# Kernel optimization log

Measured on AMD Instinct MI355X. Metric: run time of the kernel, lower is better.

The kernel has to match this reference:

```python
import jax, jax.numpy as jnp
import numpy as np

B, S, P = 2, 1024, 1024          # batch, new tokens, start_pos (cached prefix)
E, H, KV, HD = 2048, 32, 8, 64    # embed, heads, kv groups, head_dim
G = H // KV                       # group size = 4
THETA = 500000.0
CTX = P + S                       # cache/context length = 2048


def _rope_tables(start, seqlen):
    inv_freq = 1.0 / (THETA ** (jnp.arange(0, HD, 2, dtype=jnp.float32) / HD))
    pos = jnp.arange(start, start + seqlen, dtype=jnp.float32)
    freqs = jnp.outer(pos, inv_freq)              # [S, HD/2]
    emb = jnp.concatenate([freqs, freqs], axis=-1)  # [S, HD]
    return jnp.cos(emb), jnp.sin(emb)


def setup_inputs() -> dict:
    key = jax.random.key(0)
    ks = jax.random.split(key, 8)
    x = jax.random.normal(ks[0], (B, S, E), dtype=jnp.float32)
    cos1, sin1 = _rope_tables(P, S)
    cos = jnp.broadcast_to(cos1[None], (B, S, HD))
    sin = jnp.broadcast_to(sin1[None], (B, S, HD))
    # causal-with-offset additive mask: query i (global pos P+i) sees key j <= P+i
    qpos = P + jnp.arange(S)[:, None]
    kpos = jnp.arange(CTX)[None, :]
    mask = jnp.where(kpos <= qpos, 0.0, -1e9).astype(jnp.float32)[None, None]  # [1,1,S,CTX]
    cache_k = jax.random.normal(ks[1], (B, KV, CTX, HD), dtype=jnp.float32)
    cache_v = jax.random.normal(ks[2], (B, KV, CTX, HD), dtype=jnp.float32)
    sc = 0.02
    Wq = jax.random.normal(ks[3], (E, E), dtype=jnp.float32) * sc
    Wk = jax.random.normal(ks[4], (KV * HD, E), dtype=jnp.float32) * sc
    Wv = jax.random.normal(ks[5], (KV * HD, E), dtype=jnp.float32) * sc
    Wo = jax.random.normal(ks[6], (E, E), dtype=jnp.float32) * sc
    return {"x": x, "cos": cos, "sin": sin, "mask": mask,
            "cache_k": cache_k, "cache_v": cache_v,
            "Wq": Wq, "Wk": Wk, "Wv": Wv, "Wo": Wo, "start_pos": P}


def _rotate_half(t):
    t1, t2 = t[..., : HD // 2], t[..., HD // 2:]
    return jnp.concatenate([-t2, t1], axis=-1)


def _apply_rope(t, cos, sin):
    # t: [B, nh, S, HD]; cos/sin: [B, S, HD] -> unsqueeze head dim
    c = cos[:, None]
    s = sin[:, None]
    return t * c + _rotate_half(t) * s


def reference(x, cos, sin, mask, cache_k, cache_v, Wq, Wk, Wv, Wo, start_pos):
    b, s, e = x.shape
    q = (x @ Wq.T).reshape(b, s, H, HD).transpose(0, 2, 1, 3)    # [B,H,S,HD]
    k = (x @ Wk.T).reshape(b, s, KV, HD).transpose(0, 2, 1, 3)   # [B,KV,S,HD]
    v = (x @ Wv.T).reshape(b, s, KV, HD).transpose(0, 2, 1, 3)
    q = _apply_rope(q, cos, sin)
    k = _apply_rope(k, cos, sin)
    ck = cache_k.at[:, :, start_pos:start_pos + s].set(k)
    cv = cache_v.at[:, :, start_pos:start_pos + s].set(v)
    keys = ck[:, :, : start_pos + s]      # [B,KV,T,HD]
    vals = cv[:, :, : start_pos + s]
    # GQA without materializing repeated KV: view q as [B,KV,G,S,HD]
    qg = q.reshape(b, KV, G, s, HD)
    scores = jnp.einsum("bkgsh,bkth->bkgst", qg, keys) / jnp.sqrt(jnp.float32(HD))
    scores = scores + mask[:, :, None]    # broadcast mask over group dim
    probs = jax.nn.softmax(scores.astype(jnp.float32), axis=-1).astype(x.dtype)
    out = jnp.einsum("bkgst,bkth->bkgsh", probs, vals)            # [B,KV,G,S,HD]
    out = out.reshape(b, H, s, HD).transpose(0, 2, 1, 3).reshape(b, s, e)
    return out @ Wo.T
```

## Files before the change

kernel.cpp:

```cpp
#include <hip/hip_runtime.h>
#include <cstddef>

#define B   2
#define S   1024
#define PP  1024
#define CTX 2048
#define E   2048
#define H   32
#define KVH 8
#define HD  64
#define GQ  4
#define NQKV 3072

typedef short s4v  __attribute__((ext_vector_type(4)));
typedef short s8v  __attribute__((ext_vector_type(8)));
typedef float f4v  __attribute__((ext_vector_type(4)));

__device__ __forceinline__ short f2bf(float f) {
  union { float f; unsigned u; } v; v.f = f;
  unsigned r = v.u + 0x7fffu + ((v.u >> 16) & 1u);
  return (short)(r >> 16);
}
__device__ __forceinline__ float bf2f(short h) {
  union { unsigned u; float f; } v; v.u = ((unsigned)(unsigned short)h) << 16;
  return v.f;
}

__device__ __forceinline__ void gl_lds16(const void* g, void* l) {
  __builtin_amdgcn_global_load_lds((const __attribute__((address_space(1))) unsigned*)g,
                                   (__attribute__((address_space(3))) unsigned*)l, 16, 0, 0);
}

__global__ __launch_bounds__(256) void prep(const float* __restrict__ x,
                                            const float* __restrict__ Wq,
                                            const float* __restrict__ Wk,
                                            const float* __restrict__ Wv,
                                            const float* __restrict__ Wo,
                                            const float* __restrict__ ck,
                                            const float* __restrict__ cv,
                                            short* __restrict__ xb,
                                            short* __restrict__ wqkv,
                                            short* __restrict__ wob,
                                            short* __restrict__ keys,
                                            short* __restrict__ vt,
                                            float4* __restrict__ outz) {
  __shared__ short Ts[64][72];
  const int blk = blockIdx.x, tid = threadIdx.x;
  if (blk < 7168) {
    const float* s; short* d; int base;
    if (blk < 2048)      { s = x;  d = xb;             base = blk; }
    else if (blk < 4096) { s = Wq; d = wqkv;           base = blk - 2048; }
    else if (blk < 4608) { s = Wk; d = wqkv + 4194304; base = blk - 4096; }
    else if (blk < 5120) { s = Wv; d = wqkv + 5242880; base = blk - 4608; }
    else                 { s = Wo; d = wob;            base = blk - 5120; }
    int i = (base * 256 + tid) * 8;
    float4 a = *(const float4*)&s[i];
    float4 b = *(const float4*)&s[i + 4];
    s8v o;
    o[0]=f2bf(a.x); o[1]=f2bf(a.y); o[2]=f2bf(a.z); o[3]=f2bf(a.w);
    o[4]=f2bf(b.x); o[5]=f2bf(b.y); o[6]=f2bf(b.z); o[7]=f2bf(b.w);
    *(s8v*)&d[i] = o;
  } else if (blk < 7680) {
    int idx = (blk - 7168) * 256 + tid;
    int bkv = idx >> 13;
    int rem = idx & 8191;
    size_t off = (size_t)bkv * (CTX * HD) + (size_t)rem * 8;
    float4 a = *(const float4*)&ck[off];
    float4 b = *(const float4*)&ck[off + 4];
    s8v o;
    o[0]=f2bf(a.x); o[1]=f2bf(a.y); o[2]=f2bf(a.z); o[3]=f2bf(a.w);
    o[4]=f2bf(b.x); o[5]=f2bf(b.y); o[6]=f2bf(b.z); o[7]=f2bf(b.w);
    *(s8v*)&keys[off] = o;
  } else if (blk < 7936) {
    const int blk2 = blk - 7680;
    const int bkv = blk2 >> 4;
    const int p0  = (blk2 & 15) * 64;
    const float* src = cv + (size_t)bkv * CTX * HD + (size_t)p0 * HD;
    {
      int dq = tid & 15, kb = tid >> 4;
      float4 vv[4];
#pragma unroll
      for (int i = 0; i < 4; i++)
        vv[i] = *(const float4*)&src[(size_t)(kb * 4 + i) * HD + dq * 4];
#pragma unroll
      for (int j = 0; j < 4; j++) {
        s4v p;
        p[0]=f2bf(((const float*)&vv[0])[j]); p[1]=f2bf(((const float*)&vv[1])[j]);
        p[2]=f2bf(((const float*)&vv[2])[j]); p[3]=f2bf(((const float*)&vv[3])[j]);
        *(s4v*)&Ts[dq * 4 + j][kb * 4] = p;
      }
    }
    __syncthreads();
    {
      int d = tid >> 2, c = tid & 3;
      short* dst = vt + ((size_t)bkv * HD + d) * CTX + p0 + (c >> 1) * 32 + (c & 1) * 4;
#pragma unroll
      for (int j = 0; j < 4; j++) {
        s4v q4 = *(const s4v*)&Ts[d][c * 16 + j * 4];
        *(s4v*)&dst[j * 8] = q4;
      }
    }
  } else {
    int i0 = (blk - 7936) * 1024 + tid * 4;
#pragma unroll
    for (int j = 0; j < 4; j++) outz[i0 + j] = make_float4(0.f, 0.f, 0.f, 0.f);
  }
}

__global__ __launch_bounds__(256) void qkv_gemm(const short* __restrict__ A,
                                                const short* __restrict__ Bw,
                                                short* __restrict__ qb,
                                                short* __restrict__ ktmp,
                                                short* __restrict__ vt) {
  __shared__ short As[8192];
  __shared__ short Bs[8192];
  const int tid  = threadIdx.x;
  const int wv   = tid >> 6, lane = tid & 63;
  const int wm   = wv & 1, wn = wv >> 1;
  const int n16  = lane & 15, g = lane >> 4;
  const int m0   = blockIdx.y * 128, n0 = blockIdx.x * 128;
  const int K = 2048;

  const int rr = tid >> 3;
  const int cc = ((tid & 7) ^ (rr & 7)) * 8;
  const short* pA = A  + (size_t)(m0 + rr) * K + cc;
  const short* pB = Bw + (size_t)(n0 + rr) * K + cc;

  f4v acc[4][4] = {};
  for (int k0 = 0; k0 < K; k0 += 64) {
    __syncthreads();
#pragma unroll
    for (int st = 0; st < 4; st++) {
      gl_lds16(pA + (size_t)st * 32 * K, As + (st * 256 + wv * 64) * 8);
      gl_lds16(pB + (size_t)st * 32 * K, Bs + (st * 256 + wv * 64) * 8);
    }
    pA += 64; pB += 64;
    __syncthreads();

#pragma unroll
    for (int kk = 0; kk < 2; kk++) {
      s8v af[4], bf[4];
#pragma unroll
      for (int mt = 0; mt < 4; mt++)
        af[mt] = *(const s8v*)&As[(wm * 64 + mt * 16 + n16) * 64 + (((kk << 2) | g) ^ (n16 & 7)) * 8];
#pragma unroll
      for (int nt = 0; nt < 4; nt++)
        bf[nt] = *(const s8v*)&Bs[(wn * 64 + nt * 16 + n16) * 64 + (((kk << 2) | g) ^ (n16 & 7)) * 8];
#pragma unroll
      for (int mt = 0; mt < 4; mt++)
#pragma unroll
        for (int nt = 0; nt < 4; nt++)
          acc[mt][nt] = __builtin_amdgcn_mfma_f32_16x16x32_bf16(af[mt], bf[nt], acc[mt][nt], 0, 0, 0);
    }
  }

  const int rowb = m0 + wm * 64 + g * 4;
  const int colb = n0 + wn * 64 + n16;
  if (n0 < 2048) {
#pragma unroll
    for (int mt = 0; mt < 4; mt++)
#pragma unroll
      for (int nt = 0; nt < 4; nt++) {
        size_t base = (size_t)(rowb + mt * 16) * E + colb + nt * 16;
#pragma unroll
        for (int r = 0; r < 4; r++)
          qb[base + (size_t)r * E] = f2bf(acc[mt][nt][r]);
      }
  } else if (n0 < 2560) {
#pragma unroll
    for (int mt = 0; mt < 4; mt++)
#pragma unroll
      for (int nt = 0; nt < 4; nt++) {
        size_t base = (size_t)(rowb + mt * 16) * 512 + colb - 2048 + nt * 16;
#pragma unroll
        for (int r = 0; r < 4; r++)
          ktmp[base + (size_t)r * 512] = f2bf(acc[mt][nt][r]);
      }
  } else {
    const int b    = m0 >> 10;
    const int head = ((n0 - 2560) >> 6) + wn;
    const int sbase = (m0 - (b << 10)) + wm * 64;
    const size_t vrowb = (size_t)(b * KVH + head) * HD;
#pragma unroll
    for (int mt = 0; mt < 4; mt++) {
      const int pos = PP + sbase + ((mt >> 1) << 5) + ((mt & 1) << 2) + (g << 3);
#pragma unroll
      for (int nt = 0; nt < 4; nt++) {
        const int d = nt * 16 + n16;
        s4v o;
        o[0] = f2bf(acc[mt][nt][0]); o[1] = f2bf(acc[mt][nt][1]);
        o[2] = f2bf(acc[mt][nt][2]); o[3] = f2bf(acc[mt][nt][3]);
        *(s4v*)&vt[(vrowb + d) * CTX + pos] = o;
      }
    }
  }
}

__global__ __launch_bounds__(256) void gemm_bf16_sk(const short* __restrict__ A,
                                                    const short* __restrict__ Bw,
                                                    float* __restrict__ C,
                                                    int M, int N, int K) {
  __shared__ short As[8192];
  __shared__ short Bs[8192];
  const int tid  = threadIdx.x;
  const int wv   = tid >> 6, lane = tid & 63;
  const int wm   = wv & 1, wn = wv >> 1;
  const int n16  = lane & 15, g = lane >> 4;
  const int m0   = blockIdx.y * 128, n0 = blockIdx.x * 128;
  const int kh   = K >> 1;
  const int kbeg = blockIdx.z * kh;

  const int rr = tid >> 3;
  const int cc = ((tid & 7) ^ (rr & 7)) * 8;
  const short* pA = A  + (size_t)(m0 + rr) * K + kbeg + cc;
  const short* pB = Bw + (size_t)(n0 + rr) * K + kbeg + cc;

  f4v acc[4][4] = {};
  for (int k0 = 0; k0 < kh; k0 += 64) {
    __syncthreads();
#pragma unroll
    for (int st = 0; st < 4; st++) {
      gl_lds16(pA + (size_t)st * 32 * K, As + (st * 256 + wv * 64) * 8);
      gl_lds16(pB + (size_t)st * 32 * K, Bs + (st * 256 + wv * 64) * 8);
    }
    pA += 64; pB += 64;
    __syncthreads();

#pragma unroll
    for (int kk = 0; kk < 2; kk++) {
      s8v af[4], bf[4];
#pragma unroll
      for (int mt = 0; mt < 4; mt++)
        af[mt] = *(const s8v*)&As[(wm * 64 + mt * 16 + n16) * 64 + (((kk << 2) | g) ^ (n16 & 7)) * 8];
#pragma unroll
      for (int nt = 0; nt < 4; nt++)
        bf[nt] = *(const s8v*)&Bs[(wn * 64 + nt * 16 + n16) * 64 + (((kk << 2) | g) ^ (n16 & 7)) * 8];
#pragma unroll
      for (int mt = 0; mt < 4; mt++)
#pragma unroll
        for (int nt = 0; nt < 4; nt++)
          acc[mt][nt] = __builtin_amdgcn_mfma_f32_16x16x32_bf16(af[mt], bf[nt], acc[mt][nt], 0, 0, 0);
    }
  }

#pragma unroll
  for (int mt = 0; mt < 4; mt++)
#pragma unroll
    for (int nt = 0; nt < 4; nt++) {
      size_t base = (size_t)(m0 + wm * 64 + mt * 16 + g * 4) * N + n0 + wn * 64 + nt * 16 + n16;
#pragma unroll
      for (int r = 0; r < 4; r++)
        unsafeAtomicAdd(&C[base + (size_t)r * N], acc[mt][nt][r]);
    }
}

__global__ __launch_bounds__(256) void rope_kb(const short* __restrict__ ktmp,
                                               const float* __restrict__ cosb,
                                               const float* __restrict__ sinb,
                                               short* __restrict__ keys) {
  int idx = blockIdx.x * 256 + threadIdx.x;
  int d = idx & 31;
  int kv = (idx >> 5) & (KVH - 1);
  int s = (idx >> 8) & (S - 1);
  int b = idx >> 18;
  size_t row = (size_t)b * S + s;
  float c = cosb[row * HD + d];
  float sn = sinb[row * HD + d];
  float k1 = bf2f(ktmp[row * 512 + kv * 64 + d]);
  float k2 = bf2f(ktmp[row * 512 + kv * 64 + d + 32]);
  size_t drow = (((size_t)b * KVH + kv) * CTX + PP + s) * HD;
  keys[drow + d]      = f2bf(k1 * c - k2 * sn);
  keys[drow + d + 32] = f2bf(k2 * c + k1 * sn);
}

__global__ __launch_bounds__(256) void attn_mfma(const short* __restrict__ qb,
                                                 const float* __restrict__ cosb,
                                                 const float* __restrict__ sinb,
                                                 const short* __restrict__ keys,
                                                 const short* __restrict__ valsT,
                                                 short* __restrict__ attn) {
  __shared__ short Ks[8192];
  __shared__ short VTs[8192];

  const int sblk = 15 - (blockIdx.x & 15);
  const int h    = (blockIdx.x >> 4) & (H - 1);
  const int b    = blockIdx.x >> 9;
  const int kv   = h >> 2;
  const int sq0  = sblk * 64;
  const int kend = PP + sq0 + 64;

  const int tid  = threadIdx.x;
  const int w    = tid >> 6;
  const int lane = tid & 63;
  const int n    = lane & 15;
  const int g    = lane >> 4;

  const short* kbase = keys  + ((size_t)b * KVH + kv) * CTX * HD;
  const short* vtb   = valsT + ((size_t)b * KVH + kv) * (size_t)HD * CTX;

  union { s4v h4[2]; s8v v; } qlo, qhi;
  {
    const size_t row = (size_t)b * S + sq0 + w * 16 + n;
    const short* qrow = qb + row * E + h * 64;
    const float* crow = cosb + row * HD;
    const float* srow = sinb + row * HD;
    const float SC = 0.18033688011112042f;
    s8v q0 = *(const s8v*)&qrow[g * 8];
    s8v q1 = *(const s8v*)&qrow[32 + g * 8];
    float cc[8], ss[8];
    *(float4*)&cc[0] = *(const float4*)&crow[g * 8];
    *(float4*)&cc[4] = *(const float4*)&crow[g * 8 + 4];
    *(float4*)&ss[0] = *(const float4*)&srow[g * 8];
    *(float4*)&ss[4] = *(const float4*)&srow[g * 8 + 4];
#pragma unroll
    for (int j = 0; j < 8; j++) {
      float fl = bf2f(q0[j]), fh = bf2f(q1[j]);
      qlo.v[j] = f2bf((fl * cc[j] - fh * ss[j]) * SC);
      qhi.v[j] = f2bf((fh * cc[j] + fl * ss[j]) * SC);
    }
  }

  f4v O[4] = {{0,0,0,0},{0,0,0,0},{0,0,0,0},{0,0,0,0}};
  float la[4] = {0.f, 0.f, 0.f, 0.f};
  const int qp     = PP + sq0 + w * 16 + n;
  const int qmin_w = PP + sq0 + w * 16;

  const int lrow = lane >> 3;
  const int sw   = (lane & 7) ^ lrow;
  const short* kg0 = kbase + (size_t)(w * 8 + lrow) * HD + sw * 8;
  const short* kg1 = kg0 + 32 * HD;
  const short* vg0 = vtb + (size_t)(w * 8 + lrow) * CTX + sw * 8;
  const short* vg1 = vg0 + (size_t)32 * CTX;

  const int xsl = (g ^ (n & 7)) * 8;

  {
    short* kl = Ks  + w * 512;
    short* vl = VTs + w * 512;
    gl_lds16(kg0, kl);
    gl_lds16(kg1, kl + 2048);
    gl_lds16(vg0, vl);
    gl_lds16(vg1, vl + 2048);
  }

  int cur = 0;
  for (int k0 = 0; k0 < kend; k0 += 64) {
    __syncthreads();
    if (k0 + 64 < kend) {
      const int kn = k0 + 64;
      short* kl = Ks  + (cur ^ 1) * 4096 + w * 512;
      short* vl = VTs + (cur ^ 1) * 4096 + w * 512;
      gl_lds16(kg0 + (size_t)kn * HD, kl);
      gl_lds16(kg1 + (size_t)kn * HD, kl + 2048);
      gl_lds16(vg0 + kn, vl);
      gl_lds16(vg1 + kn, vl + 2048);
    }

    if (k0 < qmin_w + 16) {
      const short* kb = &Ks[cur * 4096];
      const short* vb = &VTs[cur * 4096];

      f4v sc[4];
#pragma unroll
      for (int st = 0; st < 4; st++) {
        const short* krow = kb + (st * 16 + n) * 64;
        s8v alo = *(const s8v*)(krow + xsl);
        s8v ahi = *(const s8v*)(krow + (xsl ^ 32));
        f4v z = {0.f, 0.f, 0.f, 0.f};
        z = __builtin_amdgcn_mfma_f32_16x16x32_bf16(alo, qlo.v, z, 0, 0, 0);
        sc[st] = __builtin_amdgcn_mfma_f32_16x16x32_bf16(ahi, qhi.v, z, 0, 0, 0);
      }

      if (k0 + 63 > qmin_w) {
#pragma unroll
        for (int st = 0; st < 4; st++)
#pragma unroll
          for (int r = 0; r < 4; r++) {
            int kpos = k0 + st * 16 + g * 4 + r;
            if (kpos > qp) sc[st][r] = -3e38f;
          }
      }

      union { unsigned u[4]; s8v v; } pb0, pb1;
#pragma unroll
      for (int st = 0; st < 4; st++) {
        float e0 = __builtin_amdgcn_exp2f(sc[st][0]);
        float e1 = __builtin_amdgcn_exp2f(sc[st][1]);
        float e2 = __builtin_amdgcn_exp2f(sc[st][2]);
        float e3 = __builtin_amdgcn_exp2f(sc[st][3]);
        la[0] += e0; la[1] += e1; la[2] += e2; la[3] += e3;
        unsigned w0, w1;
        asm("v_cvt_pk_bf16_f32 %0, %1, %2" : "=v"(w0) : "v"(e0), "v"(e1));
        asm("v_cvt_pk_bf16_f32 %0, %1, %2" : "=v"(w1) : "v"(e2), "v"(e3));
        if (st < 2) { pb0.u[st * 2] = w0; pb0.u[st * 2 + 1] = w1; }
        else        { pb1.u[(st - 2) * 2] = w0; pb1.u[(st - 2) * 2 + 1] = w1; }
      }

#pragma unroll
      for (int dg = 0; dg < 4; dg++) {
        const short* vr = vb + (dg * 16 + n) * 64;
        s8v va = *(const s8v*)(vr + xsl);
        s8v vx = *(const s8v*)(vr + (xsl ^ 32));
        O[dg] = __builtin_amdgcn_mfma_f32_16x16x32_bf16(va, pb0.v, O[dg], 0, 0, 0);
        O[dg] = __builtin_amdgcn_mfma_f32_16x16x32_bf16(vx, pb1.v, O[dg], 0, 0, 0);
      }
    }
    cur ^= 1;
  }

  float l = (la[0] + la[1]) + (la[2] + la[3]);
  l += __shfl_xor(l, 16);
  l += __shfl_xor(l, 32);
  const float rl = 1.f / l;
  short* orow = attn + ((size_t)b * S + sq0 + w * 16 + n) * E + h * 64;
#pragma unroll
  for (int dg = 0; dg < 4; dg++) {
    s4v o;
    o[0] = f2bf(O[dg][0] * rl); o[1] = f2bf(O[dg][1] * rl);
    o[2] = f2bf(O[dg][2] * rl); o[3] = f2bf(O[dg][3] * rl);
    *(s4v*)&orow[dg * 16 + g * 4] = o;
  }
}

extern "C" void kernel_launch(void* const* d_in, const int* in_sizes, int n_in,
                              void* d_out, int out_size, void* d_ws, size_t ws_size,
                              hipStream_t stream) {
  const float* x       = (const float*)d_in[0];
  const float* cosb    = (const float*)d_in[1];
  const float* sinb    = (const float*)d_in[2];
  const float* cache_k = (const float*)d_in[4];
  const float* cache_v = (const float*)d_in[5];
  const float* Wq      = (const float*)d_in[6];
  const float* Wk      = (const float*)d_in[7];
  const float* Wv      = (const float*)d_in[8];
  const float* Wo      = (const float*)d_in[9];
  float* out = (float*)d_out;

  short* xb    = (short*)d_ws;
  short* wqkv  = xb + 4194304;
  short* wob   = wqkv + 6291456;
  short* keysb = wob + 4194304;
  short* valsT = keysb + 2097152;
  short* aout  = valsT + 2097152;
  short* qb    = aout + 4194304;
  short* ktmp  = qb + 4194304;

  dim3 blk(256);

  prep<<<8960, blk, 0, stream>>>(x, Wq, Wk, Wv, Wo, cache_k, cache_v,
                                 xb, wqkv, wob, keysb, valsT, (float4*)out);

  qkv_gemm<<<dim3(NQKV / 128, (B * S) / 128), blk, 0, stream>>>(xb, wqkv, qb, ktmp, valsT);

  rope_kb<<<(B * S * KVH * 32) / 256, blk, 0, stream>>>(ktmp, cosb, sinb, keysb);

  attn_mfma<<<B * H * (S / 64), blk, 0, stream>>>(qb, cosb, sinb, keysb, valsT, aout);

  gemm_bf16_sk<<<dim3(E / 128, (B * S) / 128, 2), blk, 0, stream>>>(aout, wob, out, B * S, E, E);
}
```

Before: 270.8 us.

## Double-buffer GEMM LDS tiles, fuse K RoPE into QKV epilogue, single-buffer attention

Both GEMM kernels now use double-buffered LDS: the next K tile is loaded asynchronously while the current one is fed to MFMA, and the loop keeps one barrier instead of two. The K-projection epilogue of the QKV GEMM applies RoPE directly and writes into the key cache, which removes the separate rope_kb kernel and the ktmp round trip. The attention kernel does the opposite: it drops its double buffering for a single LDS buffer with load-then-sync. This halves its shared memory, likely to raise occupancy, but the K/V load latency is no longer hidden behind compute.

```diff
diff --git a/kernel.cpp b/kernel.cpp
--- a/kernel.cpp
+++ b/kernel.cpp
@@ -109,11 +109,13 @@
 
 __global__ __launch_bounds__(256) void qkv_gemm(const short* __restrict__ A,
                                                 const short* __restrict__ Bw,
+                                                const float* __restrict__ cosb,
+                                                const float* __restrict__ sinb,
                                                 short* __restrict__ qb,
-                                                short* __restrict__ ktmp,
+                                                short* __restrict__ keys,
                                                 short* __restrict__ vt) {
-  __shared__ short As[8192];
-  __shared__ short Bs[8192];
+  __shared__ short As[2][8192];
+  __shared__ short Bs[2][8192];
   const int tid  = threadIdx.x;
   const int wv   = tid >> 6, lane = tid & 63;
   const int wm   = wv & 1, wn = wv >> 1;
@@ -126,32 +128,37 @@
   const short* pA = A  + (size_t)(m0 + rr) * K + cc;
   const short* pB = Bw + (size_t)(n0 + rr) * K + cc;
 
+  auto stage = [&](int buf, int kofs) {
+#pragma unroll
+    for (int st = 0; st < 4; st++) {
+      gl_lds16(pA + kofs + (size_t)st * 32 * K, &As[buf][(st * 256 + wv * 64) * 8]);
+      gl_lds16(pB + kofs + (size_t)st * 32 * K, &Bs[buf][(st * 256 + wv * 64) * 8]);
+    }
+  };
+
   f4v acc[4][4] = {};
+  stage(0, 0);
+  int cur = 0;
   for (int k0 = 0; k0 < K; k0 += 64) {
     __syncthreads();
-#pragma unroll
-    for (int st = 0; st < 4; st++) {
-      gl_lds16(pA + (size_t)st * 32 * K, As + (st * 256 + wv * 64) * 8);
-      gl_lds16(pB + (size_t)st * 32 * K, Bs + (st * 256 + wv * 64) * 8);
-    }
-    pA += 64; pB += 64;
-    __syncthreads();
+    if (k0 + 64 < K) stage(cur ^ 1, k0 + 64);
 
 #pragma unroll
     for (int kk = 0; kk < 2; kk++) {
       s8v af[4], bf[4];
 #pragma unroll
       for (int mt = 0; mt < 4; mt++)
-        af[mt] = *(const s8v*)&As[(wm * 64 + mt * 16 + n16) * 64 + (((kk << 2) | g) ^ (n16 & 7)) * 8];
+        af[mt] = *(const s8v*)&As[cur][(wm * 64 + mt * 16 + n16) * 64 + (((kk << 2) | g) ^ (n16 & 7)) * 8];
 #pragma unroll
       for (int nt = 0; nt < 4; nt++)
-        bf[nt] = *(const s8v*)&Bs[(wn * 64 + nt * 16 + n16) * 64 + (((kk << 2) | g) ^ (n16 & 7)) * 8];
+        bf[nt] = *(const s8v*)&Bs[cur][(wn * 64 + nt * 16 + n16) * 64 + (((kk << 2) | g) ^ (n16 & 7)) * 8];
 #pragma unroll
       for (int mt = 0; mt < 4; mt++)
 #pragma unroll
         for (int nt = 0; nt < 4; nt++)
           acc[mt][nt] = __builtin_amdgcn_mfma_f32_16x16x32_bf16(af[mt], bf[nt], acc[mt][nt], 0, 0, 0);
     }
+    cur ^= 1;
   }
 
   const int rowb = m0 + wm * 64 + g * 4;
@@ -167,15 +174,27 @@
           qb[base + (size_t)r * E] = f2bf(acc[mt][nt][r]);
       }
   } else if (n0 < 2560) {
-#pragma unroll
-    for (int mt = 0; mt < 4; mt++)
-#pragma unroll
-      for (int nt = 0; nt < 4; nt++) {
-        size_t base = (size_t)(rowb + mt * 16) * 512 + colb - 2048 + nt * 16;
-#pragma unroll
-        for (int r = 0; r < 4; r++)
-          ktmp[base + (size_t)r * 512] = f2bf(acc[mt][nt][r]);
+    const int kvh = ((n0 - 2048) >> 6) + wn;
+#pragma unroll
+    for (int mt = 0; mt < 4; mt++) {
+      const int row = rowb + mt * 16;
+      const int bb = row >> 10, s = row & 1023;
+      const float* crow = cosb + ((size_t)bb * S + s) * HD;
+      const float* srow = sinb + ((size_t)bb * S + s) * HD;
+      const size_t kdst = (((size_t)bb * KVH + kvh) * CTX + PP + s) * HD;
+#pragma unroll
+      for (int nt = 0; nt < 2; nt++) {
+        const int d = n16 + nt * 16;
+#pragma unroll
+        for (int r = 0; r < 4; r++) {
+          float c  = crow[r * HD + d];
+          float sn = srow[r * HD + d];
+          float k1 = acc[mt][nt][r], k2 = acc[mt][nt + 2][r];
+          keys[kdst + (size_t)r * HD + d]      = f2bf(k1 * c - k2 * sn);
+          keys[kdst + (size_t)r * HD + d + 32] = f2bf(k2 * c + k1 * sn);
+        }
       }
+    }
   } else {
     const int b    = m0 >> 10;
     const int head = ((n0 - 2560) >> 6) + wn;
@@ -200,8 +219,8 @@
                                                     const short* __restrict__ Bw,
                                                     float* __restrict__ C,
                                                     int M, int N, int K) {
-  __shared__ short As[8192];
-  __shared__ short Bs[8192];
+  __shared__ short As[2][8192];
+  __shared__ short Bs[2][8192];
   const int tid  = threadIdx.x;
   const int wv   = tid >> 6, lane = tid & 63;
   const int wm   = wv & 1, wn = wv >> 1;
@@ -215,32 +234,37 @@
   const short* pA = A  + (size_t)(m0 + rr) * K + kbeg + cc;
   const short* pB = Bw + (size_t)(n0 + rr) * K + kbeg + cc;
 
+  auto stage = [&](int buf, int kofs) {
+#pragma unroll
+    for (int st = 0; st < 4; st++) {
+      gl_lds16(pA + kofs + (size_t)st * 32 * K, &As[buf][(st * 256 + wv * 64) * 8]);
+      gl_lds16(pB + kofs + (size_t)st * 32 * K, &Bs[buf][(st * 256 + wv * 64) * 8]);
+    }
+  };
+
   f4v acc[4][4] = {};
+  stage(0, 0);
+  int cur = 0;
   for (int k0 = 0; k0 < kh; k0 += 64) {
     __syncthreads();
-#pragma unroll
-    for (int st = 0; st < 4; st++) {
-      gl_lds16(pA + (size_t)st * 32 * K, As + (st * 256 + wv * 64) * 8);
-      gl_lds16(pB + (size_t)st * 32 * K, Bs + (st * 256 + wv * 64) * 8);
-    }
-    pA += 64; pB += 64;
-    __syncthreads();
+    if (k0 + 64 < kh) stage(cur ^ 1, k0 + 64);
 
 #pragma unroll
     for (int kk = 0; kk < 2; kk++) {
       s8v af[4], bf[4];
 #pragma unroll
       for (int mt = 0; mt < 4; mt++)
-        af[mt] = *(const s8v*)&As[(wm * 64 + mt * 16 + n16) * 64 + (((kk << 2) | g) ^ (n16 & 7)) * 8];
+        af[mt] = *(const s8v*)&As[cur][(wm * 64 + mt * 16 + n16) * 64 + (((kk << 2) | g) ^ (n16 & 7)) * 8];
 #pragma unroll
       for (int nt = 0; nt < 4; nt++)
-        bf[nt] = *(const s8v*)&Bs[(wn * 64 + nt * 16 + n16) * 64 + (((kk << 2) | g) ^ (n16 & 7)) * 8];
+        bf[nt] = *(const s8v*)&Bs[cur][(wn * 64 + nt * 16 + n16) * 64 + (((kk << 2) | g) ^ (n16 & 7)) * 8];
 #pragma unroll
       for (int mt = 0; mt < 4; mt++)
 #pragma unroll
         for (int nt = 0; nt < 4; nt++)
           acc[mt][nt] = __builtin_amdgcn_mfma_f32_16x16x32_bf16(af[mt], bf[nt], acc[mt][nt], 0, 0, 0);
     }
+    cur ^= 1;
   }
 
 #pragma unroll
@@ -252,25 +276,6 @@
       for (int r = 0; r < 4; r++)
         unsafeAtomicAdd(&C[base + (size_t)r * N], acc[mt][nt][r]);
     }
-}
-
-__global__ __launch_bounds__(256) void rope_kb(const short* __restrict__ ktmp,
-                                               const float* __restrict__ cosb,
-                                               const float* __restrict__ sinb,
-                                               short* __restrict__ keys) {
-  int idx = blockIdx.x * 256 + threadIdx.x;
-  int d = idx & 31;
-  int kv = (idx >> 5) & (KVH - 1);
-  int s = (idx >> 8) & (S - 1);
-  int b = idx >> 18;
-  size_t row = (size_t)b * S + s;
-  float c = cosb[row * HD + d];
-  float sn = sinb[row * HD + d];
-  float k1 = bf2f(ktmp[row * 512 + kv * 64 + d]);
-  float k2 = bf2f(ktmp[row * 512 + kv * 64 + d + 32]);
-  size_t drow = (((size_t)b * KVH + kv) * CTX + PP + s) * HD;
-  keys[drow + d]      = f2bf(k1 * c - k2 * sn);
-  keys[drow + d + 32] = f2bf(k2 * c + k1 * sn);
 }
 
 __global__ __launch_bounds__(256) void attn_mfma(const short* __restrict__ qb,
@@ -279,8 +284,8 @@
                                                  const short* __restrict__ keys,
                                                  const short* __restrict__ valsT,
                                                  short* __restrict__ attn) {
-  __shared__ short Ks[8192];
-  __shared__ short VTs[8192];
+  __shared__ short Ks[4096];
+  __shared__ short VTs[4096];
 
   const int sblk = 15 - (blockIdx.x & 15);
   const int h    = (blockIdx.x >> 4) & (H - 1);
@@ -331,81 +336,67 @@
   const short* kg1 = kg0 + 32 * HD;
   const short* vg0 = vtb + (size_t)(w * 8 + lrow) * CTX + sw * 8;
   const short* vg1 = vg0 + (size_t)32 * CTX;
+  short* kl0 = Ks + w * 512;
+  short* kl1 = Ks + 2048 + w * 512;
+  short* vl0 = VTs + w * 512;
+  short* vl1 = VTs + 2048 + w * 512;
 
   const int xsl = (g ^ (n & 7)) * 8;
 
-  {
-    short* kl = Ks  + w * 512;
-    short* vl = VTs + w * 512;
-    gl_lds16(kg0, kl);
-    gl_lds16(kg1, kl + 2048);
-    gl_lds16(vg0, vl);
-    gl_lds16(vg1, vl + 2048);
-  }
-
-  int cur = 0;
   for (int k0 = 0; k0 < kend; k0 += 64) {
     __syncthreads();
-    if (k0 + 64 < kend) {
-      const int kn = k0 + 64;
-      short* kl = Ks  + (cur ^ 1) * 4096 + w * 512;
-      short* vl = VTs + (cur ^ 1) * 4096 + w * 512;
-      gl_lds16(kg0 + (size_t)kn * HD, kl);
-      gl_lds16(kg1 + (size_t)kn * HD, kl + 2048);
-      gl_lds16(vg0 + kn, vl);
-      gl_lds16(vg1 + kn, vl + 2048);
-    }
-
-    if (k0 < qmin_w + 16) {
-      const short* kb = &Ks[cur * 4096];
-      const short* vb = &VTs[cur * 4096];
-
-      f4v sc[4];
-#pragma unroll
-      for (int st = 0; st < 4; st++) {
-        const short* krow = kb + (st * 16 + n) * 64;
-        s8v alo = *(const s8v*)(krow + xsl);
-        s8v ahi = *(const s8v*)(krow + (xsl ^ 32));
-        f4v z = {0.f, 0.f, 0.f, 0.f};
-        z = __builtin_amdgcn_mfma_f32_16x16x32_bf16(alo, qlo.v, z, 0, 0, 0);
-        sc[st] = __builtin_amdgcn_mfma_f32_16x16x32_bf16(ahi, qhi.v, z, 0, 0, 0);
-      }
-
-      if (k0 + 63 > qmin_w) {
-#pragma unroll
-        for (int st = 0; st < 4; st++)
-#pragma unroll
-          for (int r = 0; r < 4; r++) {
-            int kpos = k0 + st * 16 + g * 4 + r;
-            if (kpos > qp) sc[st][r] = -3e38f;
-          }
-      }
-
-      union { unsigned u[4]; s8v v; } pb0, pb1;
-#pragma unroll
-      for (int st = 0; st < 4; st++) {
-        float e0 = __builtin_amdgcn_exp2f(sc[st][0]);
-        float e1 = __builtin_amdgcn_exp2f(sc[st][1]);
-        float e2 = __builtin_amdgcn_exp2f(sc[st][2]);
-        float e3 = __builtin_amdgcn_exp2f(sc[st][3]);
-        la[0] += e0; la[1] += e1; la[2] += e2; la[3] += e3;
-        unsigned w0, w1;
-        asm("v_cvt_pk_bf16_f32 %0, %1, %2" : "=v"(w0) : "v"(e0), "v"(e1));
-        asm("v_cvt_pk_bf16_f32 %0, %1, %2" : "=v"(w1) : "v"(e2), "v"(e3));
-        if (st < 2) { pb0.u[st * 2] = w0; pb0.u[st * 2 + 1] = w1; }
-        else        { pb1.u[(st - 2) * 2] = w0; pb1.u[(st - 2) * 2 + 1] = w1; }
-      }
-
-#pragma unroll
-      for (int dg = 0; dg < 4; dg++) {
-        const short* vr = vb + (dg * 16 + n) * 64;
-        s8v va = *(const s8v*)(vr + xsl);
-        s8v vx = *(const s8v*)(vr + (xsl ^ 32));
-        O[dg] = __builtin_amdgcn_mfma_f32_16x16x32_bf16(va, pb0.v, O[dg], 0, 0, 0);
-        O[dg] = __builtin_amdgcn_mfma_f32_16x16x32_bf16(vx, pb1.v, O[dg], 0, 0, 0);
-      }
-    }
-    cur ^= 1;
+    gl_lds16(kg0 + (size_t)k0 * HD, kl0);
+    gl_lds16(kg1 + (size_t)k0 * HD, kl1);
+    gl_lds16(vg0 + k0, vl0);
+    gl_lds16(vg1 + k0, vl1);
+    __syncthreads();
+
+    if (k0 >= qmin_w + 16) continue;
+
+    f4v sc[4];
+#pragma unroll
+    for (int st = 0; st < 4; st++) {
+      const short* krow = &Ks[(st * 16 + n) * 64];
+      s8v alo = *(const s8v*)(krow + xsl);
+      s8v ahi = *(const s8v*)(krow + (xsl ^ 32));
+      f4v z = {0.f, 0.f, 0.f, 0.f};
+      z = __builtin_amdgcn_mfma_f32_16x16x32_bf16(alo, qlo.v, z, 0, 0, 0);
+      sc[st] = __builtin_amdgcn_mfma_f32_16x16x32_bf16(ahi, qhi.v, z, 0, 0, 0);
+    }
+
+    if (k0 + 63 > qmin_w) {
+#pragma unroll
+      for (int st = 0; st < 4; st++)
+#pragma unroll
+        for (int r = 0; r < 4; r++) {
+          int kpos = k0 + st * 16 + g * 4 + r;
+          if (kpos > qp) sc[st][r] = -3e38f;
+        }
+    }
+
+    union { unsigned u[4]; s8v v; } pb0, pb1;
+#pragma unroll
+    for (int st = 0; st < 4; st++) {
+      float e0 = __builtin_amdgcn_exp2f(sc[st][0]);
+      float e1 = __builtin_amdgcn_exp2f(sc[st][1]);
+      float e2 = __builtin_amdgcn_exp2f(sc[st][2]);
+      float e3 = __builtin_amdgcn_exp2f(sc[st][3]);
+      la[0] += e0; la[1] += e1; la[2] += e2; la[3] += e3;
+      unsigned w0, w1;
+      asm("v_cvt_pk_bf16_f32 %0, %1, %2" : "=v"(w0) : "v"(e0), "v"(e1));
+      asm("v_cvt_pk_bf16_f32 %0, %1, %2" : "=v"(w1) : "v"(e2), "v"(e3));
+      if (st < 2) { pb0.u[st * 2] = w0; pb0.u[st * 2 + 1] = w1; }
+      else        { pb1.u[(st - 2) * 2] = w0; pb1.u[(st - 2) * 2 + 1] = w1; }
+    }
+
+#pragma unroll
+    for (int dg = 0; dg < 4; dg++) {
+      const short* vr = &VTs[(dg * 16 + n) * 64];
+      s8v va = *(const s8v*)(vr + xsl);
+      s8v vx = *(const s8v*)(vr + (xsl ^ 32));
+      O[dg] = __builtin_amdgcn_mfma_f32_16x16x32_bf16(va, pb0.v, O[dg], 0, 0, 0);
+      O[dg] = __builtin_amdgcn_mfma_f32_16x16x32_bf16(vx, pb1.v, O[dg], 0, 0, 0);
+    }
   }
 
   float l = (la[0] + la[1]) + (la[2] + la[3]);
@@ -443,16 +434,14 @@
   short* valsT = keysb + 2097152;
   short* aout  = valsT + 2097152;
   short* qb    = aout + 4194304;
-  short* ktmp  = qb + 4194304;
 
   dim3 blk(256);
 
   prep<<<8960, blk, 0, stream>>>(x, Wq, Wk, Wv, Wo, cache_k, cache_v,
                                  xb, wqkv, wob, keysb, valsT, (float4*)out);
 
-  qkv_gemm<<<dim3(NQKV / 128, (B * S) / 128), blk, 0, stream>>>(xb, wqkv, qb, ktmp, valsT);
-
-  rope_kb<<<(B * S * KVH * 32) / 256, blk, 0, stream>>>(ktmp, cosb, sinb, keysb);
+  qkv_gemm<<<dim3(NQKV / 128, (B * S) / 128), blk, 0, stream>>>(xb, wqkv, cosb, sinb,
+                                                                qb, keysb, valsT);
 
   attn_mfma<<<B * H * (S / 64), blk, 0, stream>>>(qb, cosb, sinb, keysb, valsT, aout);
 
```

After: 259.3 us. 1.04x faster.
